# Performance work log

Measured on AMD Instinct MI355X. Metric: run time of the kernel, lower is better.

## Reference

```python
import jax, jax.numpy as jnp
import numpy as np

B, IN, OUT, FAN = 2048, 4096, 4096, 64

def setup_inputs() -> dict:
    key = jax.random.key(0)
    k1, k2, k3, k4 = jax.random.split(key, 4)
    input = jax.random.normal(k1, (B, IN), dtype=jnp.float32)
    condensed_weight = jax.random.normal(k2, (OUT, FAN), dtype=jnp.float32) * 0.05
    bias = jax.random.normal(k3, (OUT,), dtype=jnp.float32) * 0.05
    input_mask = jax.random.randint(k4, (OUT, FAN), 0, IN, dtype=jnp.int64)
    return {"input": input, "condensed_weight": condensed_weight,
            "bias": bias, "input_mask": input_mask}

def reference(input, condensed_weight, bias, input_mask):
    # Per output neuron o: sum_f input[b, idx[o,f]] * w[o,f] + bias[o]
    # gathered: [B, OUT, FAN] -- the structured-sparse gather
    gathered = jnp.take(input, input_mask, axis=1)
    return jnp.einsum("bof,of->bo", gathered, condensed_weight) + bias
```

## Files before the change

### kernel.cpp

```cpp
#include <hip/hip_runtime.h>

#define B_DIM   2048
#define IN_DIM  4096
#define OUT_DIM 4096
#define FAN     64


typedef float v2f __attribute__((ext_vector_type(2)));

__device__ __forceinline__ unsigned bf16_rne(float f) {
    unsigned u = __float_as_uint(f);
    return (u + 0x7fffu + ((u >> 16) & 1u)) >> 16;
}

__global__ __launch_bounds__(256) void pack_kernel(
    const float* __restrict__ input, uint4* __restrict__ wsp)
{
    const int idx = blockIdx.x * 256 + threadIdx.x;
    const int t   = idx >> 11;
    const int c0  = (idx & 2047) << 1;

    const float* p = input + (size_t)t * 4 * IN_DIM + c0;
    const float2 r0 = *reinterpret_cast<const float2*>(p + 0 * IN_DIM);
    const float2 r1 = *reinterpret_cast<const float2*>(p + 1 * IN_DIM);
    const float2 r2 = *reinterpret_cast<const float2*>(p + 2 * IN_DIM);
    const float2 r3 = *reinterpret_cast<const float2*>(p + 3 * IN_DIM);

    uint4 q;
    q.x = bf16_rne(r0.x) | (bf16_rne(r1.x) << 16);
    q.y = bf16_rne(r2.x) | (bf16_rne(r3.x) << 16);
    q.z = bf16_rne(r0.y) | (bf16_rne(r1.y) << 16);
    q.w = bf16_rne(r2.y) | (bf16_rne(r3.y) << 16);

    wsp[(size_t)t * 2048 + (c0 >> 1)] = q;
}

__global__ __launch_bounds__(256, 2) void condensed_kernel(
    const uint4* __restrict__ wsp,
    const float* __restrict__ weight,
    const float* __restrict__ bias,
    const int*   __restrict__ mask,
    float*       __restrict__ out)
{
    __shared__ __align__(16) uint4 lds[4096];

    const int tid   = threadIdx.x;
    const int o     = blockIdx.y * 256 + tid;
    const int bseg  = blockIdx.x * 64;
    const int tbase = bseg >> 2;

    unsigned addrs[FAN];
    float    wv[FAN];
    {
        const int4*   mv = reinterpret_cast<const int4*>(mask)     + o * (FAN / 4);
        const float4* wp = reinterpret_cast<const float4*>(weight) + o * (FAN / 4);
        #pragma unroll
        for (int j = 0; j < FAN / 4; ++j) {
            int4   m4 = mv[j];
            float4 w4 = wp[j];
            addrs[4*j+0] = (unsigned)m4.x << 3;
            addrs[4*j+1] = (unsigned)m4.y << 3;
            addrs[4*j+2] = (unsigned)m4.z << 3;
            addrs[4*j+3] = (unsigned)m4.w << 3;
            wv[4*j+0] = w4.x;
            wv[4*j+1] = w4.y;
            wv[4*j+2] = w4.z;
            wv[4*j+3] = w4.w;
        }
    }
    const float bv = bias[o];

    {
        const uint4* src = wsp + (size_t)tbase * 2048 + tid;
        #pragma unroll
        for (int it = 0; it < 8; ++it) {
            __builtin_amdgcn_global_load_lds(
                (const __attribute__((address_space(1))) unsigned*)(src + it * 256),
                (__attribute__((address_space(3))) unsigned*)(lds + it * 256 + tid),
                16, 0, 0);
        }
    }
    __syncthreads();

    const char* ldsb = reinterpret_cast<const char*>(lds);

    for (int hp = 0; hp < 8; ++hp) {
        const int h0 = hp * 2;

        {
            const uint4* src = wsp + (size_t)(tbase + h0 + 1) * 2048 + tid;
            #pragma unroll
            for (int it = 0; it < 8; ++it) {
                __builtin_amdgcn_global_load_lds(
                    (const __attribute__((address_space(1))) unsigned*)(src + it * 256),
                    (__attribute__((address_space(3))) unsigned*)(lds + 2048 + it * 256 + tid),
                    16, 0, 0);
            }
        }
        {
            v2f a01 = {0.f, 0.f}, a23 = {0.f, 0.f};
            #pragma unroll
            for (int j = 0; j < FAN; ++j) {
                const uint2 g = *reinterpret_cast<const uint2*>(ldsb + addrs[j]);
                const v2f w2 = {wv[j], wv[j]};
                v2f v;
                v.x = __uint_as_float(g.x << 16);
                v.y = __uint_as_float(g.x & 0xffff0000u);
                a01 = __builtin_elementwise_fma(v, w2, a01);
                v.x = __uint_as_float(g.y << 16);
                v.y = __uint_as_float(g.y & 0xffff0000u);
                a23 = __builtin_elementwise_fma(v, w2, a23);
            }
            float* op = out + (size_t)(bseg + 4 * h0) * OUT_DIM + o;
            op[0 * OUT_DIM] = a01.x + bv;
            op[1 * OUT_DIM] = a01.y + bv;
            op[2 * OUT_DIM] = a23.x + bv;
            op[3 * OUT_DIM] = a23.y + bv;
        }
        __syncthreads();

        if (hp < 7) {
            const uint4* src = wsp + (size_t)(tbase + h0 + 2) * 2048 + tid;
            #pragma unroll
            for (int it = 0; it < 8; ++it) {
                __builtin_amdgcn_global_load_lds(
                    (const __attribute__((address_space(1))) unsigned*)(src + it * 256),
                    (__attribute__((address_space(3))) unsigned*)(lds + it * 256 + tid),
                    16, 0, 0);
            }
        }
        {
            v2f a01 = {0.f, 0.f}, a23 = {0.f, 0.f};
            #pragma unroll
            for (int j = 0; j < FAN; ++j) {
                const uint2 g = *reinterpret_cast<const uint2*>(ldsb + 32768 + addrs[j]);
                const v2f w2 = {wv[j], wv[j]};
                v2f v;
                v.x = __uint_as_float(g.x << 16);
                v.y = __uint_as_float(g.x & 0xffff0000u);
                a01 = __builtin_elementwise_fma(v, w2, a01);
                v.x = __uint_as_float(g.y << 16);
                v.y = __uint_as_float(g.y & 0xffff0000u);
                a23 = __builtin_elementwise_fma(v, w2, a23);
            }
            float* op = out + (size_t)(bseg + 4 * h0 + 4) * OUT_DIM + o;
            op[0 * OUT_DIM] = a01.x + bv;
            op[1 * OUT_DIM] = a01.y + bv;
            op[2 * OUT_DIM] = a23.x + bv;
            op[3 * OUT_DIM] = a23.y + bv;
        }
        __syncthreads();
    }
}

extern "C" void kernel_launch(void* const* d_in, const int* in_sizes, int n_in,
                              void* d_out, int out_size, void* d_ws, size_t ws_size,
                              hipStream_t stream) {
    const float* input  = (const float*)d_in[0];
    const float* weight = (const float*)d_in[1];
    const float* bias   = (const float*)d_in[2];
    const int*   mask   = (const int*)d_in[3];
    float*       out    = (float*)d_out;
    uint4*       wsp    = (uint4*)d_ws;

    pack_kernel<<<4096, 256, 0, stream>>>(input, wsp);
    dim3 grid(32, 16);
    condensed_kernel<<<grid, 256, 0, stream>>>(wsp, weight, bias, mask, out);
}
```

Measured before the change: 129.6 us.

## Pack eight batch rows per bf16 tile and use 1024-thread blocks

The pack kernel now interleaves 8 batch rows per column into one 16-byte bf16 vector instead of 4. The main kernel uses 1024-thread blocks covering 1024 outputs, with 64KB double-buffered LDS tiles, and each thread reads a 16-byte gather giving 8 FMAs pairs per index. This cuts redundant reloads of each input tile across output blocks and halves the number of LDS gather instructions per output. In exchange, the grid shrinks to 256 blocks of 1024 threads using 128KB LDS each, which means one block per CU. The aggressive launch bounds may force the compiler to spill the 128 per-thread index and weight registers.

```diff
diff --git a/kernel.cpp b/kernel.cpp
--- a/kernel.cpp
+++ b/kernel.cpp
@@ -20,34 +20,39 @@
     const int t   = idx >> 11;
     const int c0  = (idx & 2047) << 1;
 
-    const float* p = input + (size_t)t * 4 * IN_DIM + c0;
-    const float2 r0 = *reinterpret_cast<const float2*>(p + 0 * IN_DIM);
-    const float2 r1 = *reinterpret_cast<const float2*>(p + 1 * IN_DIM);
-    const float2 r2 = *reinterpret_cast<const float2*>(p + 2 * IN_DIM);
-    const float2 r3 = *reinterpret_cast<const float2*>(p + 3 * IN_DIM);
+    const float* p = input + (size_t)t * 8 * IN_DIM + c0;
+    float2 r[8];
+    #pragma unroll
+    for (int i = 0; i < 8; ++i)
+        r[i] = *reinterpret_cast<const float2*>(p + i * IN_DIM);
 
-    uint4 q;
-    q.x = bf16_rne(r0.x) | (bf16_rne(r1.x) << 16);
-    q.y = bf16_rne(r2.x) | (bf16_rne(r3.x) << 16);
-    q.z = bf16_rne(r0.y) | (bf16_rne(r1.y) << 16);
-    q.w = bf16_rne(r2.y) | (bf16_rne(r3.y) << 16);
+    uint4 q0, q1;
+    q0.x = bf16_rne(r[0].x) | (bf16_rne(r[1].x) << 16);
+    q0.y = bf16_rne(r[2].x) | (bf16_rne(r[3].x) << 16);
+    q0.z = bf16_rne(r[4].x) | (bf16_rne(r[5].x) << 16);
+    q0.w = bf16_rne(r[6].x) | (bf16_rne(r[7].x) << 16);
+    q1.x = bf16_rne(r[0].y) | (bf16_rne(r[1].y) << 16);
+    q1.y = bf16_rne(r[2].y) | (bf16_rne(r[3].y) << 16);
+    q1.z = bf16_rne(r[4].y) | (bf16_rne(r[5].y) << 16);
+    q1.w = bf16_rne(r[6].y) | (bf16_rne(r[7].y) << 16);
 
-    wsp[(size_t)t * 2048 + (c0 >> 1)] = q;
+    wsp[(size_t)t * 4096 + c0 + 0] = q0;
+    wsp[(size_t)t * 4096 + c0 + 1] = q1;
 }
 
-__global__ __launch_bounds__(256, 2) void condensed_kernel(
+__global__ __launch_bounds__(1024, 4) void condensed_kernel(
     const uint4* __restrict__ wsp,
     const float* __restrict__ weight,
     const float* __restrict__ bias,
     const int*   __restrict__ mask,
     float*       __restrict__ out)
 {
-    __shared__ __align__(16) uint4 lds[4096];
+    __shared__ __align__(16) uint4 lds[8192];
 
-    const int tid   = threadIdx.x;
-    const int o     = blockIdx.y * 256 + tid;
-    const int bseg  = blockIdx.x * 64;
-    const int tbase = bseg >> 2;
+    const int tid     = threadIdx.x;
+    const int o       = blockIdx.y * 1024 + tid;
+    const int tbase   = blockIdx.x * 4;
+    const int rowbase = blockIdx.x * 32;
 
     unsigned addrs[FAN];
     float    wv[FAN];
@@ -58,10 +63,10 @@
         for (int j = 0; j < FAN / 4; ++j) {
             int4   m4 = mv[j];
             float4 w4 = wp[j];
-            addrs[4*j+0] = (unsigned)m4.x << 3;
-            addrs[4*j+1] = (unsigned)m4.y << 3;
-            addrs[4*j+2] = (unsigned)m4.z << 3;
-            addrs[4*j+3] = (unsigned)m4.w << 3;
+            addrs[4*j+0] = (unsigned)m4.x << 4;
+            addrs[4*j+1] = (unsigned)m4.y << 4;
+            addrs[4*j+2] = (unsigned)m4.z << 4;
+            addrs[4*j+3] = (unsigned)m4.w << 4;
             wv[4*j+0] = w4.x;
             wv[4*j+1] = w4.y;
             wv[4*j+2] = w4.z;
@@ -71,12 +76,12 @@
     const float bv = bias[o];
 
     {
-        const uint4* src = wsp + (size_t)tbase * 2048 + tid;
+        const uint4* src = wsp + (size_t)tbase * 4096 + tid;
         #pragma unroll
-        for (int it = 0; it < 8; ++it) {
+        for (int it = 0; it < 4; ++it) {
             __builtin_amdgcn_global_load_lds(
-                (const __attribute__((address_space(1))) unsigned*)(src + it * 256),
-                (__attribute__((address_space(3))) unsigned*)(lds + it * 256 + tid),
+                (const __attribute__((address_space(1))) unsigned*)(src + it * 1024),
+                (__attribute__((address_space(3))) unsigned*)(lds + it * 1024 + tid),
                 16, 0, 0);
         }
     }
@@ -84,24 +89,26 @@
 
     const char* ldsb = reinterpret_cast<const char*>(lds);
 
-    for (int hp = 0; hp < 8; ++hp) {
-        const int h0 = hp * 2;
-
-        {
-            const uint4* src = wsp + (size_t)(tbase + h0 + 1) * 2048 + tid;
+    #pragma unroll
+    for (int p = 0; p < 4; ++p) {
+        if (p < 3) {
+            const uint4* src = wsp + (size_t)(tbase + p + 1) * 4096 + tid;
+            const int bufo = ((p + 1) & 1) * 4096;
             #pragma unroll
-            for (int it = 0; it < 8; ++it) {
+            for (int it = 0; it < 4; ++it) {
                 __builtin_amdgcn_global_load_lds(
-                    (const __attribute__((address_space(1))) unsigned*)(src + it * 256),
-                    (__attribute__((address_space(3))) unsigned*)(lds + 2048 + it * 256 + tid),
+                    (const __attribute__((address_space(1))) unsigned*)(src + it * 1024),
+                    (__attribute__((address_space(3))) unsigned*)(lds + bufo + it * 1024 + tid),
                     16, 0, 0);
             }
         }
+
         {
-            v2f a01 = {0.f, 0.f}, a23 = {0.f, 0.f};
+            const char* base = ldsb + (p & 1) * 65536;
+            v2f a01 = {0.f, 0.f}, a23 = {0.f, 0.f}, a45 = {0.f, 0.f}, a67 = {0.f, 0.f};
             #pragma unroll
             for (int j = 0; j < FAN; ++j) {
-                const uint2 g = *reinterpret_cast<const uint2*>(ldsb + addrs[j]);
+                const uint4 g = *reinterpret_cast<const uint4*>(base + addrs[j]);
                 const v2f w2 = {wv[j], wv[j]};
                 v2f v;
                 v.x = __uint_as_float(g.x << 16);
@@ -110,46 +117,26 @@
                 v.x = __uint_as_float(g.y << 16);
                 v.y = __uint_as_float(g.y & 0xffff0000u);
                 a23 = __builtin_elementwise_fma(v, w2, a23);
+                v.x = __uint_as_float(g.z << 16);
+                v.y = __uint_as_float(g.z & 0xffff0000u);
+                a45 = __builtin_elementwise_fma(v, w2, a45);
+                v.x = __uint_as_float(g.w << 16);
+                v.y = __uint_as_float(g.w & 0xffff0000u);
+                a67 = __builtin_elementwise_fma(v, w2, a67);
             }
-            float* op = out + (size_t)(bseg + 4 * h0) * OUT_DIM + o;
+
+            float* op = out + (size_t)(rowbase + 8 * p) * OUT_DIM + o;
             op[0 * OUT_DIM] = a01.x + bv;
             op[1 * OUT_DIM] = a01.y + bv;
             op[2 * OUT_DIM] = a23.x + bv;
             op[3 * OUT_DIM] = a23.y + bv;
+            op[4 * OUT_DIM] = a45.x + bv;
+            op[5 * OUT_DIM] = a45.y + bv;
+            op[6 * OUT_DIM] = a67.x + bv;
+            op[7 * OUT_DIM] = a67.y + bv;
         }
-        __syncthreads();
 
-        if (hp < 7) {
-            const uint4* src = wsp + (size_t)(tbase + h0 + 2) * 2048 + tid;
-            #pragma unroll
-            for (int it = 0; it < 8; ++it) {
-                __builtin_amdgcn_global_load_lds(
-                    (const __attribute__((address_space(1))) unsigned*)(src + it * 256),
-                    (__attribute__((address_space(3))) unsigned*)(lds + it * 256 + tid),
-                    16, 0, 0);
-            }
-        }
-        {
-            v2f a01 = {0.f, 0.f}, a23 = {0.f, 0.f};
-            #pragma unroll
-            for (int j = 0; j < FAN; ++j) {
-                const uint2 g = *reinterpret_cast<const uint2*>(ldsb + 32768 + addrs[j]);
-                const v2f w2 = {wv[j], wv[j]};
-                v2f v;
-                v.x = __uint_as_float(g.x << 16);
-                v.y = __uint_as_float(g.x & 0xffff0000u);
-                a01 = __builtin_elementwise_fma(v, w2, a01);
-                v.x = __uint_as_float(g.y << 16);
-                v.y = __uint_as_float(g.y & 0xffff0000u);
-                a23 = __builtin_elementwise_fma(v, w2, a23);
-            }
-            float* op = out + (size_t)(bseg + 4 * h0 + 4) * OUT_DIM + o;
-            op[0 * OUT_DIM] = a01.x + bv;
-            op[1 * OUT_DIM] = a01.y + bv;
-            op[2 * OUT_DIM] = a23.x + bv;
-            op[3 * OUT_DIM] = a23.y + bv;
-        }
-        __syncthreads();
+        if (p < 3) __syncthreads();
     }
 }
 
@@ -163,7 +150,7 @@
     float*       out    = (float*)d_out;
     uint4*       wsp    = (uint4*)d_ws;
 
-    pack_kernel<<<4096, 256, 0, stream>>>(input, wsp);
-    dim3 grid(32, 16);
-    condensed_kernel<<<grid, 256, 0, stream>>>(wsp, weight, bias, mask, out);
+    pack_kernel<<<2048, 256, 0, stream>>>(input, wsp);
+    dim3 grid(64, 4);
+    condensed_kernel<<<grid, 1024, 0, stream>>>(wsp, weight, bias, mask, out);
 }
```

After: 184.0 us. 1.42x slower.

## Replace double-buffered LDS pipeline with single buffer and double the grid

Applied to the files above, without the earlier changes.

Drops the two-slot LDS double buffering and uses a single 32KB buffer that is loaded and then synchronised before each 4-row tile is computed. Each block now handles 32 batch rows instead of 64, and the grid doubles to 64x16 blocks. The smaller LDS footprint allows more resident blocks per CU, so load/compute overlap comes from occupancy rather than in-block prefetch. The trade-off is that every block must reload the mask and weights and exposes its load latency before each tile.

```diff
diff --git a/kernel.cpp b/kernel.cpp
--- a/kernel.cpp
+++ b/kernel.cpp
@@ -42,12 +42,12 @@
     const int*   __restrict__ mask,
     float*       __restrict__ out)
 {
-    __shared__ __align__(16) uint4 lds[4096];
+    __shared__ __align__(16) uint4 lds[2048];
 
-    const int tid   = threadIdx.x;
-    const int o     = blockIdx.y * 256 + tid;
-    const int bseg  = blockIdx.x * 64;
-    const int tbase = bseg >> 2;
+    const int tid     = threadIdx.x;
+    const int o       = blockIdx.y * 256 + tid;
+    const int tbase   = blockIdx.x * 8;
+    const int rowbase = blockIdx.x * 32;
 
     unsigned addrs[FAN];
     float    wv[FAN];
@@ -70,33 +70,23 @@
     }
     const float bv = bias[o];
 
-    {
-        const uint4* src = wsp + (size_t)tbase * 2048 + tid;
-        #pragma unroll
-        for (int it = 0; it < 8; ++it) {
-            __builtin_amdgcn_global_load_lds(
-                (const __attribute__((address_space(1))) unsigned*)(src + it * 256),
-                (__attribute__((address_space(3))) unsigned*)(lds + it * 256 + tid),
-                16, 0, 0);
-        }
-    }
-    __syncthreads();
-
     const char* ldsb = reinterpret_cast<const char*>(lds);
 
-    for (int hp = 0; hp < 8; ++hp) {
-        const int h0 = hp * 2;
+    for (int t = 0; t < 8; ++t) {
+        if (t) __syncthreads();
 
         {
-            const uint4* src = wsp + (size_t)(tbase + h0 + 1) * 2048 + tid;
+            const uint4* src = wsp + (size_t)(tbase + t) * 2048 + tid;
             #pragma unroll
             for (int it = 0; it < 8; ++it) {
                 __builtin_amdgcn_global_load_lds(
                     (const __attribute__((address_space(1))) unsigned*)(src + it * 256),
-                    (__attribute__((address_space(3))) unsigned*)(lds + 2048 + it * 256 + tid),
+                    (__attribute__((address_space(3))) unsigned*)(lds + it * 256 + tid),
                     16, 0, 0);
             }
         }
+        __syncthreads();
+
         {
             v2f a01 = {0.f, 0.f}, a23 = {0.f, 0.f};
             #pragma unroll
@@ -111,45 +101,12 @@
                 v.y = __uint_as_float(g.y & 0xffff0000u);
                 a23 = __builtin_elementwise_fma(v, w2, a23);
             }
-            float* op = out + (size_t)(bseg + 4 * h0) * OUT_DIM + o;
+            float* op = out + (size_t)(rowbase + 4 * t) * OUT_DIM + o;
             op[0 * OUT_DIM] = a01.x + bv;
             op[1 * OUT_DIM] = a01.y + bv;
             op[2 * OUT_DIM] = a23.x + bv;
             op[3 * OUT_DIM] = a23.y + bv;
         }
-        __syncthreads();
-
-        if (hp < 7) {
-            const uint4* src = wsp + (size_t)(tbase + h0 + 2) * 2048 + tid;
-            #pragma unroll
-            for (int it = 0; it < 8; ++it) {
-                __builtin_amdgcn_global_load_lds(
-                    (const __attribute__((address_space(1))) unsigned*)(src + it * 256),
-                    (__attribute__((address_space(3))) unsigned*)(lds + it * 256 + tid),
-                    16, 0, 0);
-            }
-        }
-        {
-            v2f a01 = {0.f, 0.f}, a23 = {0.f, 0.f};
-            #pragma unroll
-            for (int j = 0; j < FAN; ++j) {
-                const uint2 g = *reinterpret_cast<const uint2*>(ldsb + 32768 + addrs[j]);
-                const v2f w2 = {wv[j], wv[j]};
-                v2f v;
-                v.x = __uint_as_float(g.x << 16);
-                v.y = __uint_as_float(g.x & 0xffff0000u);
-                a01 = __builtin_elementwise_fma(v, w2, a01);
-                v.x = __uint_as_float(g.y << 16);
-                v.y = __uint_as_float(g.y & 0xffff0000u);
-                a23 = __builtin_elementwise_fma(v, w2, a23);
-            }
-            float* op = out + (size_t)(bseg + 4 * h0 + 4) * OUT_DIM + o;
-            op[0 * OUT_DIM] = a01.x + bv;
-            op[1 * OUT_DIM] = a01.y + bv;
-            op[2 * OUT_DIM] = a23.x + bv;
-            op[3 * OUT_DIM] = a23.y + bv;
-        }
-        __syncthreads();
     }
 }
 
@@ -164,6 +121,6 @@
     uint4*       wsp    = (uint4*)d_ws;
 
     pack_kernel<<<4096, 256, 0, stream>>>(input, wsp);
-    dim3 grid(32, 16);
+    dim3 grid(64, 16);
     condensed_kernel<<<grid, 256, 0, stream>>>(wsp, weight, bias, mask, out);
 }
```

After: 134.7 us. +3.9%, slower.

## Pack two batch rows per bf16 word and double grid of condensed kernel

Applied to the files above, without the earlier changes.

The packing changes from four batch rows per 8-byte entry to two rows per 4-byte word. Each LDS stage now holds 16 KB covering two rows, the LDS footprint halves, and the grid doubles along the batch dimension. The aim is more resident blocks and more parallel blocks, which should hide gather latency. In exchange, mask and weight registers are reloaded in twice as many blocks, each LDS read yields half as many FMAs, and the launch-bounds occupancy hint is dropped.

```diff
diff --git a/kernel.cpp b/kernel.cpp
--- a/kernel.cpp
+++ b/kernel.cpp
@@ -17,37 +17,35 @@
     const float* __restrict__ input, uint4* __restrict__ wsp)
 {
     const int idx = blockIdx.x * 256 + threadIdx.x;
-    const int t   = idx >> 11;
-    const int c0  = (idx & 2047) << 1;
+    const int t   = idx >> 10;
+    const int c0  = (idx & 1023) << 2;
 
-    const float* p = input + (size_t)t * 4 * IN_DIM + c0;
-    const float2 r0 = *reinterpret_cast<const float2*>(p + 0 * IN_DIM);
-    const float2 r1 = *reinterpret_cast<const float2*>(p + 1 * IN_DIM);
-    const float2 r2 = *reinterpret_cast<const float2*>(p + 2 * IN_DIM);
-    const float2 r3 = *reinterpret_cast<const float2*>(p + 3 * IN_DIM);
+    const float* p = input + (size_t)t * 2 * IN_DIM + c0;
+    const float4 r0 = *reinterpret_cast<const float4*>(p);
+    const float4 r1 = *reinterpret_cast<const float4*>(p + IN_DIM);
 
     uint4 q;
     q.x = bf16_rne(r0.x) | (bf16_rne(r1.x) << 16);
-    q.y = bf16_rne(r2.x) | (bf16_rne(r3.x) << 16);
-    q.z = bf16_rne(r0.y) | (bf16_rne(r1.y) << 16);
-    q.w = bf16_rne(r2.y) | (bf16_rne(r3.y) << 16);
+    q.y = bf16_rne(r0.y) | (bf16_rne(r1.y) << 16);
+    q.z = bf16_rne(r0.z) | (bf16_rne(r1.z) << 16);
+    q.w = bf16_rne(r0.w) | (bf16_rne(r1.w) << 16);
 
-    wsp[(size_t)t * 2048 + (c0 >> 1)] = q;
+    wsp[idx] = q;
 }
 
-__global__ __launch_bounds__(256, 2) void condensed_kernel(
+__global__ __launch_bounds__(256) void condensed_kernel(
     const uint4* __restrict__ wsp,
     const float* __restrict__ weight,
     const float* __restrict__ bias,
     const int*   __restrict__ mask,
     float*       __restrict__ out)
 {
-    __shared__ __align__(16) uint4 lds[4096];
+    __shared__ __align__(16) uint4 lds[2048];
 
-    const int tid   = threadIdx.x;
-    const int o     = blockIdx.y * 256 + tid;
-    const int bseg  = blockIdx.x * 64;
-    const int tbase = bseg >> 2;
+    const int tid     = threadIdx.x;
+    const int o       = blockIdx.y * 256 + tid;
+    const int tbase   = blockIdx.x * 16;
+    const int rowbase = blockIdx.x * 32;
 
     unsigned addrs[FAN];
     float    wv[FAN];
@@ -58,10 +56,10 @@
         for (int j = 0; j < FAN / 4; ++j) {
             int4   m4 = mv[j];
             float4 w4 = wp[j];
-            addrs[4*j+0] = (unsigned)m4.x << 3;
-            addrs[4*j+1] = (unsigned)m4.y << 3;
-            addrs[4*j+2] = (unsigned)m4.z << 3;
-            addrs[4*j+3] = (unsigned)m4.w << 3;
+            addrs[4*j+0] = (unsigned)m4.x << 2;
+            addrs[4*j+1] = (unsigned)m4.y << 2;
+            addrs[4*j+2] = (unsigned)m4.z << 2;
+            addrs[4*j+3] = (unsigned)m4.w << 2;
             wv[4*j+0] = w4.x;
             wv[4*j+1] = w4.y;
             wv[4*j+2] = w4.z;
@@ -71,9 +69,9 @@
     const float bv = bias[o];
 
     {
-        const uint4* src = wsp + (size_t)tbase * 2048 + tid;
+        const uint4* src = wsp + (size_t)tbase * 1024 + tid;
         #pragma unroll
-        for (int it = 0; it < 8; ++it) {
+        for (int it = 0; it < 4; ++it) {
             __builtin_amdgcn_global_load_lds(
                 (const __attribute__((address_space(1))) unsigned*)(src + it * 256),
                 (__attribute__((address_space(3))) unsigned*)(lds + it * 256 + tid),
@@ -85,44 +83,37 @@
     const char* ldsb = reinterpret_cast<const char*>(lds);
 
     for (int hp = 0; hp < 8; ++hp) {
-        const int h0 = hp * 2;
-
         {
-            const uint4* src = wsp + (size_t)(tbase + h0 + 1) * 2048 + tid;
+            const uint4* src = wsp + (size_t)(tbase + 2 * hp + 1) * 1024 + tid;
             #pragma unroll
-            for (int it = 0; it < 8; ++it) {
+            for (int it = 0; it < 4; ++it) {
                 __builtin_amdgcn_global_load_lds(
                     (const __attribute__((address_space(1))) unsigned*)(src + it * 256),
-                    (__attribute__((address_space(3))) unsigned*)(lds + 2048 + it * 256 + tid),
+                    (__attribute__((address_space(3))) unsigned*)(lds + 1024 + it * 256 + tid),
                     16, 0, 0);
             }
         }
         {
-            v2f a01 = {0.f, 0.f}, a23 = {0.f, 0.f};
+            v2f a01 = {0.f, 0.f};
             #pragma unroll
             for (int j = 0; j < FAN; ++j) {
-                const uint2 g = *reinterpret_cast<const uint2*>(ldsb + addrs[j]);
+                const unsigned g = *reinterpret_cast<const unsigned*>(ldsb + addrs[j]);
                 const v2f w2 = {wv[j], wv[j]};
                 v2f v;
-                v.x = __uint_as_float(g.x << 16);
-                v.y = __uint_as_float(g.x & 0xffff0000u);
+                v.x = __uint_as_float(g << 16);
+                v.y = __uint_as_float(g & 0xffff0000u);
                 a01 = __builtin_elementwise_fma(v, w2, a01);
-                v.x = __uint_as_float(g.y << 16);
-                v.y = __uint_as_float(g.y & 0xffff0000u);
-                a23 = __builtin_elementwise_fma(v, w2, a23);
             }
-            float* op = out + (size_t)(bseg + 4 * h0) * OUT_DIM + o;
+            float* op = out + (size_t)(rowbase + 4 * hp) * OUT_DIM + o;
             op[0 * OUT_DIM] = a01.x + bv;
             op[1 * OUT_DIM] = a01.y + bv;
-            op[2 * OUT_DIM] = a23.x + bv;
-            op[3 * OUT_DIM] = a23.y + bv;
         }
         __syncthreads();
 
         if (hp < 7) {
-            const uint4* src = wsp + (size_t)(tbase + h0 + 2) * 2048 + tid;
+            const uint4* src = wsp + (size_t)(tbase + 2 * hp + 2) * 1024 + tid;
             #pragma unroll
-            for (int it = 0; it < 8; ++it) {
+            for (int it = 0; it < 4; ++it) {
                 __builtin_amdgcn_global_load_lds(
                     (const __attribute__((address_space(1))) unsigned*)(src + it * 256),
                     (__attribute__((address_space(3))) unsigned*)(lds + it * 256 + tid),
@@ -130,24 +121,19 @@
             }
         }
         {
-            v2f a01 = {0.f, 0.f}, a23 = {0.f, 0.f};
+            v2f a01 = {0.f, 0.f};
             #pragma unroll
             for (int j = 0; j < FAN; ++j) {
-                const uint2 g = *reinterpret_cast<const uint2*>(ldsb + 32768 + addrs[j]);
+                const unsigned g = *reinterpret_cast<const unsigned*>(ldsb + 16384 + addrs[j]);
                 const v2f w2 = {wv[j], wv[j]};
                 v2f v;
-                v.x = __uint_as_float(g.x << 16);
-                v.y = __uint_as_float(g.x & 0xffff0000u);
+                v.x = __uint_as_float(g << 16);
+                v.y = __uint_as_float(g & 0xffff0000u);
                 a01 = __builtin_elementwise_fma(v, w2, a01);
-                v.x = __uint_as_float(g.y << 16);
-                v.y = __uint_as_float(g.y & 0xffff0000u);
-                a23 = __builtin_elementwise_fma(v, w2, a23);
             }
-            float* op = out + (size_t)(bseg + 4 * h0 + 4) * OUT_DIM + o;
+            float* op = out + (size_t)(rowbase + 4 * hp + 2) * OUT_DIM + o;
             op[0 * OUT_DIM] = a01.x + bv;
             op[1 * OUT_DIM] = a01.y + bv;
-            op[2 * OUT_DIM] = a23.x + bv;
-            op[3 * OUT_DIM] = a23.y + bv;
         }
         __syncthreads();
     }
@@ -164,6 +150,6 @@
     uint4*       wsp    = (uint4*)d_ws;
 
     pack_kernel<<<4096, 256, 0, stream>>>(input, wsp);
-    dim3 grid(32, 16);
+    dim3 grid(64, 16);
     condensed_kernel<<<grid, 256, 0, stream>>>(wsp, weight, bias, mask, out);
 }
```

Result: slower. 158.9 us (+22.7%).
